# Performance work log

Hardware: AMD Instinct MI355X
Metric: run time of the kernel (lower is better)

## Reference

```python
import jax, jax.numpy as jnp
import numpy as np

N, E, F_IN = 10000, 160000, 256
H1, C1 = 8, 128          # conv1: heads=8, out 128 per head, concat -> 1024
H2, C2 = 1, 64           # conv2: heads=1, out 64
NEG_SLOPE = 0.2


def setup_inputs() -> dict:
    key = jax.random.key(0)
    ks = jax.random.split(key, 10)
    s_in = 1.0 / np.sqrt(F_IN)
    s_h1 = 1.0 / np.sqrt(H1 * C1)
    return {
        "x": jax.random.normal(ks[0], (N, F_IN), dtype=jnp.float32),
        "edge_index": jax.random.randint(ks[1], (2, E), 0, N, dtype=jnp.int64),
        "W1": jax.random.normal(ks[2], (F_IN, H1 * C1), dtype=jnp.float32) * s_in,
        "att_src1": jax.random.normal(ks[3], (H1, C1), dtype=jnp.float32) * 0.1,
        "att_dst1": jax.random.normal(ks[4], (H1, C1), dtype=jnp.float32) * 0.1,
        "b1": jnp.zeros((H1 * C1,), dtype=jnp.float32),
        "W2": jax.random.normal(ks[5], (H1 * C1, H2 * C2), dtype=jnp.float32) * s_h1,
        "att_src2": jax.random.normal(ks[6], (H2, C2), dtype=jnp.float32) * 0.1,
        "att_dst2": jax.random.normal(ks[7], (H2, C2), dtype=jnp.float32) * 0.1,
        "b2": jnp.zeros((H2 * C2,), dtype=jnp.float32),
    }


def gat_conv(x, src, dst, W, att_src, att_dst, b, n):
    """PyG GATConv (eval mode: dropout off), concat=True, add_self_loops handled by caller."""
    H, C = att_src.shape
    h = (x @ W).reshape(n, H, C)                       # [N,H,C]
    a_s = jnp.einsum('nhc,hc->nh', h, att_src)         # [N,H]
    a_d = jnp.einsum('nhc,hc->nh', h, att_dst)         # [N,H]
    e = jax.nn.leaky_relu(a_s[src] + a_d[dst], NEG_SLOPE)  # [Etot,H]
    # softmax over edges grouped by destination node (numerically stable)
    e_max = jax.ops.segment_max(e, dst, num_segments=n)
    e = jnp.exp(e - e_max[dst])
    denom = jax.ops.segment_sum(e, dst, num_segments=n)
    alpha = e / (denom[dst] + 1e-16)                   # [Etot,H]
    msg = h[src] * alpha[:, :, None]                   # [Etot,H,C]
    out = jax.ops.segment_sum(msg, dst, num_segments=n)  # [N,H,C]
    return out.reshape(n, H * C) + b


def reference(x, edge_index, W1, att_src1, att_dst1, b1, W2, att_src2, att_dst2, b2):
    n = x.shape[0]
    loops = jnp.arange(n, dtype=edge_index.dtype)
    src = jnp.concatenate([edge_index[0], loops])
    dst = jnp.concatenate([edge_index[1], loops])
    h = jax.nn.elu(gat_conv(x, src, dst, W1, att_src1, att_dst1, b1, n))
    return gat_conv(h, src, dst, W2, att_src2, att_dst2, b2, n)
```

## Files before the change

### kernel.cpp

```cpp
#include <hip/hip_runtime.h>
#include <cmath>


typedef short bf16x8 __attribute__((ext_vector_type(8)));
typedef float f32x4 __attribute__((ext_vector_type(4)));
typedef unsigned short u16x8 __attribute__((ext_vector_type(8)));

__device__ __forceinline__ float lrelu(float x) { return x > 0.f ? x : 0.2f * x; }
__device__ __forceinline__ float b2f(unsigned short h) {
  return __uint_as_float(((unsigned)h) << 16);
}
__device__ __forceinline__ unsigned short f2bf(float f) {
  unsigned u = __float_as_uint(f);
  u += 0x7FFFu + ((u >> 16) & 1u);
  return (unsigned short)(u >> 16);
}

__device__ __forceinline__ void fma8(float* acc, uint4 v, float e) {
  acc[0] += e * __uint_as_float(v.x << 16);
  acc[1] += e * __uint_as_float(v.x & 0xffff0000u);
  acc[2] += e * __uint_as_float(v.y << 16);
  acc[3] += e * __uint_as_float(v.y & 0xffff0000u);
  acc[4] += e * __uint_as_float(v.z << 16);
  acc[5] += e * __uint_as_float(v.z & 0xffff0000u);
  acc[6] += e * __uint_as_float(v.w << 16);
  acc[7] += e * __uint_as_float(v.w & 0xffff0000u);
}

#define GLOAD_LDS16(gsrc, ldst)                                              \
  __builtin_amdgcn_global_load_lds(                                          \
      (const __attribute__((address_space(1))) unsigned int*)(gsrc),         \
      (__attribute__((address_space(3))) unsigned int*)(ldst), 16, 0, 0)


__global__ __launch_bounds__(256) void prep_fused(
    const int* __restrict__ ei, int* __restrict__ counts, int E,
    const float* __restrict__ x, unsigned short* __restrict__ xpk, int N, int MB1,
    const float* __restrict__ W1, unsigned short* __restrict__ w1pk,
    const float* __restrict__ W2, unsigned short* __restrict__ w2pk) {
  const int countB = (E + 255) / 256;
  const int pxB = MB1 * 8;
  int bid = blockIdx.x;
  int t = threadIdx.x;

  if (bid < countB) {
    int e = bid * 256 + t;
    if (e < E) atomicAdd(&counts[ei[E + e]], 1);
    return;
  }
  bid -= countB;
  if (bid < pxB) {
    int mb = bid >> 3, ks = bid & 7;
    int l = t & 63, f = t >> 6;
    int row = mb * 64 + f * 16 + (l & 15);
    int kc = ks * 32 + (l >> 4) * 8;
    float v[8];
#pragma unroll
    for (int j = 0; j < 8; ++j) v[j] = 0.f;
    if (row < N) {
      const float* xr = x + (size_t)row * 256 + kc;
#pragma unroll
      for (int j = 0; j < 8; ++j) v[j] = xr[j];
    }
    u16x8 hi, lo;
#pragma unroll
    for (int j = 0; j < 8; ++j) {
      unsigned short h = f2bf(v[j]);
      hi[j] = h; lo[j] = f2bf(v[j] - b2f(h));
    }
    size_t base = (size_t)(mb * 8 + ks) * 8 * 512;
    *(u16x8*)(xpk + base + (size_t)f * 512 + l * 8) = hi;
    *(u16x8*)(xpk + base + (size_t)(4 + f) * 512 + l * 8) = lo;
    return;
  }
  bid -= pxB;
  if (bid < 64) {
    int hb = bid >> 3, ks = bid & 7;
    int l = t & 63, gq = t >> 6;
    for (int g = gq; g < 8; g += 4) {
      int n = hb * 128 + g * 16 + (l & 15);
      int k0 = ks * 32 + (l >> 4) * 8;
      u16x8 hi, lo;
#pragma unroll
      for (int j = 0; j < 8; ++j) {
        float v = W1[(size_t)(k0 + j) * 1024 + n];
        unsigned short h = f2bf(v);
        hi[j] = h; lo[j] = f2bf(v - b2f(h));
      }
      size_t base = (size_t)(hb * 8 + ks) * 16 * 512;
      *(u16x8*)(w1pk + base + (size_t)g * 512 + l * 8) = hi;
      *(u16x8*)(w1pk + base + (size_t)(8 + g) * 512 + l * 8) = lo;
    }
    return;
  }
  bid -= 64;
  {
    int ks = bid;
    int l = t & 63, g = t >> 6;
    int n = g * 16 + (l & 15);
    int k0 = ks * 32 + (l >> 4) * 8;
    u16x8 hi, lo;
#pragma unroll
    for (int j = 0; j < 8; ++j) {
      float v = W2[(size_t)(k0 + j) * 64 + n];
      unsigned short h = f2bf(v);
      hi[j] = h; lo[j] = f2bf(v - b2f(h));
    }
    size_t base = (size_t)ks * 8 * 512;
    *(u16x8*)(w2pk + base + (size_t)g * 512 + l * 8) = hi;
    *(u16x8*)(w2pk + base + (size_t)(4 + g) * 512 + l * 8) = lo;
  }
}


__global__ __launch_bounds__(256) void scan_blk(const int* __restrict__ counts,
                                                int* __restrict__ offsets,
                                                int* __restrict__ bsum, int n) {
  __shared__ int lds[256];
  int b = blockIdx.x, t = threadIdx.x, i = b * 256 + t;
  int v = (i < n) ? counts[i] + 1 : 0;
  lds[t] = v;
  __syncthreads();
  for (int off = 1; off < 256; off <<= 1) {
    int tv = (t >= off) ? lds[t - off] : 0;
    __syncthreads();
    lds[t] += tv;
    __syncthreads();
  }
  if (i < n) offsets[i] = lds[t] - v;
  if (t == 255) bsum[b] = lds[255];
}

__global__ __launch_bounds__(256) void scan_apply(int* __restrict__ offsets,
                                                  int* __restrict__ cursors,
                                                  const int* __restrict__ bsum,
                                                  int nb, int n) {
  __shared__ int pre_s;
  int b = blockIdx.x, t = threadIdx.x;
  if (t == 0) {
    int s = 0;
    for (int i = 0; i < b; ++i) s += bsum[i];
    pre_s = s;
    if (b == nb - 1) {
      int tot = s;
      for (int i = b; i < nb; ++i) tot += bsum[i];
      offsets[n] = tot;
    }
  }
  __syncthreads();
  int i = b * 256 + t;
  if (i < n) {
    int o = offsets[i] + pre_s;
    offsets[i] = o;
    cursors[i] = o;
  }
}

__global__ __launch_bounds__(256) void fill_all(const int* __restrict__ ei,
                                                int* __restrict__ cursors,
                                                const int* __restrict__ offsets,
                                                int* __restrict__ list,
                                                int E, int n) {
  int tid = blockIdx.x * 256 + threadIdx.x;
  if (tid < E) {
    int d = ei[E + tid];
    int pos = atomicAdd(&cursors[d], 1);
    list[pos] = ei[tid];
  } else if (tid < E + n) {
    int i = tid - E;
    list[offsets[i + 1] - 1] = i;
  }
}


__global__ __launch_bounds__(512, 4) void gemm1_att(
    const unsigned short* __restrict__ xpk, const unsigned short* __restrict__ w1pk,
    const float* __restrict__ asrc, const float* __restrict__ adst,
    unsigned short* __restrict__ h1b, float* __restrict__ as1,
    float* __restrict__ ad1) {
  extern __shared__ char sm[];
  const int t = threadIdx.x, wid = t >> 6, lane = t & 63;
  const int wr = wid >> 2, wc = wid & 3;
  const int mb = blockIdx.x, hb = blockIdx.y;
  const int m0 = mb * 128;
  const int l15 = lane & 15, l4 = lane >> 4;

  f32x4 acc[4][2] = {};

  auto stage = [&](int buf, int ks) {
    char* base0 = sm + buf * 32768;
    for (int i = wid; i < 32; i += 8) {
      const unsigned short* src;
      int ldsoff;
      if (i < 8) {
        int r = i >> 2;
        src = xpk + (size_t)((2 * mb + r) * 8 + ks) * 4096 + (i & 3) * 512 + lane * 8;
        ldsoff = i * 1024;
      } else if (i < 16) {
        int f = i - 8, r = f >> 2;
        src = xpk + (size_t)((2 * mb + r) * 8 + ks) * 4096 + (4 + (f & 3)) * 512 + lane * 8;
        ldsoff = 8192 + f * 1024;
      } else if (i < 24) {
        int g = i - 16;
        src = w1pk + (size_t)(hb * 8 + ks) * 8192 + g * 512 + lane * 8;
        ldsoff = 16384 + g * 1024;
      } else {
        int g = i - 24;
        src = w1pk + (size_t)(hb * 8 + ks) * 8192 + (8 + g) * 512 + lane * 8;
        ldsoff = 24576 + g * 1024;
      }
      GLOAD_LDS16(src, base0 + ldsoff);
    }
  };

  stage(0, 0);
  __syncthreads();
  int buf = 0;
  for (int step = 0; step < 8; ++step) {
    if (step < 7) stage(buf ^ 1, step + 1);
    const char* b = sm + buf * 32768;
    bf16x8 ah[4], al[4], bh[2], bl[2];
#pragma unroll
    for (int mf = 0; mf < 4; ++mf) {
      ah[mf] = *(const bf16x8*)(b + (wr * 4 + mf) * 1024 + lane * 16);
      al[mf] = *(const bf16x8*)(b + 8192 + (wr * 4 + mf) * 1024 + lane * 16);
    }
#pragma unroll
    for (int nf = 0; nf < 2; ++nf) {
      bh[nf] = *(const bf16x8*)(b + 16384 + (wc * 2 + nf) * 1024 + lane * 16);
      bl[nf] = *(const bf16x8*)(b + 24576 + (wc * 2 + nf) * 1024 + lane * 16);
    }
#pragma unroll
    for (int mf = 0; mf < 4; ++mf)
#pragma unroll
      for (int nf = 0; nf < 2; ++nf) {
        acc[mf][nf] = __builtin_amdgcn_mfma_f32_16x16x32_bf16(ah[mf], bh[nf], acc[mf][nf], 0, 0, 0);
        acc[mf][nf] = __builtin_amdgcn_mfma_f32_16x16x32_bf16(ah[mf], bl[nf], acc[mf][nf], 0, 0, 0);
        acc[mf][nf] = __builtin_amdgcn_mfma_f32_16x16x32_bf16(al[mf], bh[nf], acc[mf][nf], 0, 0, 0);
      }
    __syncthreads();
    buf ^= 1;
  }

  float* parts_s = (float*)sm;
  float* parts_d = (float*)(sm + 2048);
  unsigned short* ctile = (unsigned short*)(sm + 4096);
  float as_c[2], ad_c[2];
#pragma unroll
  for (int nf = 0; nf < 2; ++nf) {
    int col = hb * 128 + wc * 32 + nf * 16 + l15;
    as_c[nf] = asrc[col];
    ad_c[nf] = adst[col];
  }
#pragma unroll
  for (int mf = 0; mf < 4; ++mf) {
    float ss[4] = {0.f, 0.f, 0.f, 0.f}, dd[4] = {0.f, 0.f, 0.f, 0.f};
#pragma unroll
    for (int nf = 0; nf < 2; ++nf)
#pragma unroll
      for (int r = 0; r < 4; ++r) {
        ss[r] += acc[mf][nf][r] * as_c[nf];
        dd[r] += acc[mf][nf][r] * ad_c[nf];
      }
#pragma unroll
    for (int r = 0; r < 4; ++r)
      for (int m = 1; m < 16; m <<= 1) {
        ss[r] += __shfl_xor(ss[r], m);
        dd[r] += __shfl_xor(dd[r], m);
      }
    if (l15 == 0) {
#pragma unroll
      for (int r = 0; r < 4; ++r) {
        int row = wr * 64 + mf * 16 + l4 * 4 + r;
        parts_s[row * 4 + wc] = ss[r];
        parts_d[row * 4 + wc] = dd[r];
      }
    }
#pragma unroll
    for (int nf = 0; nf < 2; ++nf)
#pragma unroll
      for (int r = 0; r < 4; ++r) {
        int row = wr * 64 + mf * 16 + l4 * 4 + r;
        int col = wc * 32 + nf * 16 + l15;
        ctile[row * 128 + col] = f2bf(acc[mf][nf][r]);
      }
  }
  __syncthreads();
  if (t < 128) {
    float s = parts_s[t * 4] + parts_s[t * 4 + 1] + parts_s[t * 4 + 2] + parts_s[t * 4 + 3];
    float d = parts_d[t * 4] + parts_d[t * 4 + 1] + parts_d[t * 4 + 2] + parts_d[t * 4 + 3];
    as1[(size_t)(m0 + t) * 8 + hb] = s;
    ad1[(size_t)(m0 + t) * 8 + hb] = d;
  }
#pragma unroll
  for (int rep = 0; rep < 4; ++rep) {
    int e = rep * 4096 + t * 8;
    int row = e >> 7, col = e & 127;
    bf16x8 v = *(const bf16x8*)(ctile + e);
    *(bf16x8*)(h1b + (size_t)(m0 + row) * 1024 + hb * 128 + col) = v;
  }
}


__global__ __launch_bounds__(256) void agg1_gather(
    const unsigned short* __restrict__ h1b, const float* __restrict__ as1,
    const float* __restrict__ ad1, const int* __restrict__ offsets,
    const int* __restrict__ list, const float* __restrict__ b1,
    unsigned short* __restrict__ o1pk, int n) {
  __shared__ __align__(16) unsigned short stg[8192];
  const int t = threadIdx.x, w = t >> 6, lane = t & 63;
  const int node = blockIdx.x * 4 + w;
  const int h0 = lane >> 4, h1_ = h0 + 4;

  if (node < n) {
    const int beg = offsets[node], end = offsets[node + 1];
    const float ad0 = ad1[(size_t)node * 8 + h0];
    const float ad4 = ad1[(size_t)node * 8 + h1_];
    float acc0[8] = {}, acc1[8] = {};
    float den0 = 0.f, den4 = 0.f;

    int j = beg;
    int sA = 0, sB = 0;
    float aA0 = 0.f, aA4 = 0.f, aB0 = 0.f, aB4 = 0.f;
    uint4 vA0, vA1, vB0, vB1;
    if (j + 2 <= end) {
      sA = list[j]; sB = list[j + 1];
      aA0 = as1[(size_t)sA * 8 + h0]; aA4 = as1[(size_t)sA * 8 + h1_];
      aB0 = as1[(size_t)sB * 8 + h0]; aB4 = as1[(size_t)sB * 8 + h1_];
      vA0 = *(const uint4*)(h1b + (size_t)sA * 1024 + lane * 8);
      vA1 = *(const uint4*)(h1b + (size_t)sA * 1024 + 512 + lane * 8);
      vB0 = *(const uint4*)(h1b + (size_t)sB * 1024 + lane * 8);
      vB1 = *(const uint4*)(h1b + (size_t)sB * 1024 + 512 + lane * 8);
    }
    for (; j + 4 <= end; j += 2) {
      int sA2 = list[j + 2], sB2 = list[j + 3];
      float aA02 = as1[(size_t)sA2 * 8 + h0], aA42 = as1[(size_t)sA2 * 8 + h1_];
      float aB02 = as1[(size_t)sB2 * 8 + h0], aB42 = as1[(size_t)sB2 * 8 + h1_];
      uint4 nA0 = *(const uint4*)(h1b + (size_t)sA2 * 1024 + lane * 8);
      uint4 nA1 = *(const uint4*)(h1b + (size_t)sA2 * 1024 + 512 + lane * 8);
      uint4 nB0 = *(const uint4*)(h1b + (size_t)sB2 * 1024 + lane * 8);
      uint4 nB1 = *(const uint4*)(h1b + (size_t)sB2 * 1024 + 512 + lane * 8);
      float eA0 = __expf(lrelu(aA0 + ad0)), eA4 = __expf(lrelu(aA4 + ad4));
      float eB0 = __expf(lrelu(aB0 + ad0)), eB4 = __expf(lrelu(aB4 + ad4));
      den0 += eA0 + eB0; den4 += eA4 + eB4;
      fma8(acc0, vA0, eA0); fma8(acc1, vA1, eA4);
      fma8(acc0, vB0, eB0); fma8(acc1, vB1, eB4);
      sA = sA2; sB = sB2;
      aA0 = aA02; aA4 = aA42; aB0 = aB02; aB4 = aB42;
      vA0 = nA0; vA1 = nA1; vB0 = nB0; vB1 = nB1;
    }
    if (j + 2 <= end) {
      float eA0 = __expf(lrelu(aA0 + ad0)), eA4 = __expf(lrelu(aA4 + ad4));
      float eB0 = __expf(lrelu(aB0 + ad0)), eB4 = __expf(lrelu(aB4 + ad4));
      den0 += eA0 + eB0; den4 += eA4 + eB4;
      fma8(acc0, vA0, eA0); fma8(acc1, vA1, eA4);
      fma8(acc0, vB0, eB0); fma8(acc1, vB1, eB4);
      j += 2;
    }
    if (j < end) {
      int s = list[j];
      float a0 = as1[(size_t)s * 8 + h0], a4 = as1[(size_t)s * 8 + h1_];
      uint4 v0 = *(const uint4*)(h1b + (size_t)s * 1024 + lane * 8);
      uint4 v1 = *(const uint4*)(h1b + (size_t)s * 1024 + 512 + lane * 8);
      float e0 = __expf(lrelu(a0 + ad0)), e4 = __expf(lrelu(a4 + ad4));
      den0 += e0; den4 += e4;
      fma8(acc0, v0, e0); fma8(acc1, v1, e4);
    }

    const float inv0 = 1.f / (den0 + 1e-16f);
    const float inv4 = 1.f / (den4 + 1e-16f);
    u16x8 hiA, loA, hiB, loB;
#pragma unroll
    for (int k = 0; k < 8; ++k) {
      float vA = acc0[k] * inv0 + b1[lane * 8 + k];
      float vB = acc1[k] * inv4 + b1[512 + lane * 8 + k];
      vA = vA > 0.f ? vA : expm1f(vA);
      vB = vB > 0.f ? vB : expm1f(vB);
      unsigned short hA = f2bf(vA), hB = f2bf(vB);
      hiA[k] = hA; loA[k] = f2bf(vA - b2f(hA));
      hiB[k] = hB; loB[k] = f2bf(vB - b2f(hB));
    }
    const int q2 = lane >> 2, kc = lane & 3;
    {
      int aw = q2 * 512 + kc * 64 + w * 16;
      *(u16x8*)((char*)stg + (aw ^ ((q2 & 7) << 4))) = hiA;
      aw += 256;
      *(u16x8*)((char*)stg + (aw ^ ((q2 & 7) << 4))) = loA;
    }
    {
      int ks = 16 + q2;
      int aw = ks * 512 + kc * 64 + w * 16;
      *(u16x8*)((char*)stg + (aw ^ ((ks & 7) << 4))) = hiB;
      aw += 256;
      *(u16x8*)((char*)stg + (aw ^ ((ks & 7) << 4))) = loB;
    }
  }
  __syncthreads();
  const int blk = blockIdx.x;
  const int mb = blk >> 4, f = (blk >> 2) & 3, l15b = (blk & 3) * 4;
#pragma unroll
  for (int it = 0; it < 4; ++it) {
    int a = it * 4096 + t * 16;
    int ks = a >> 9, half = (a >> 8) & 1, kcc = (a >> 6) & 3, ww = (a >> 4) & 3;
    u16x8 v = *(const u16x8*)((const char*)stg + (a ^ ((ks & 7) << 4)));
    size_t g = (size_t)(mb * 32 + ks) * 4096 + half * 2048 + (size_t)f * 512 +
               (size_t)(kcc * 16 + l15b + ww) * 8;
    *(u16x8*)(o1pk + g) = v;
  }
}


__global__ __launch_bounds__(256) void gemm2_splitk(
    const unsigned short* __restrict__ o1pk, const unsigned short* __restrict__ w2pk,
    float* __restrict__ h2p, int Mpad) {
  extern __shared__ char sm[];
  const int t = threadIdx.x, wid = t >> 6, lane = t & 63;
  const int wr = wid >> 1, wc = wid & 1;
  const int mb = blockIdx.x, sk = blockIdx.y;
  const int m0 = mb * 64;
  const int l15 = lane & 15, l4 = lane >> 4;

  f32x4 acc[2][2] = {};

  auto stage = [&](int buf, int ks) {
    char* base0 = sm + buf * 16384;
    const unsigned short* ax = o1pk + (size_t)(mb * 32 + ks) * 8 * 512 + lane * 8;
    for (int i = wid; i < 8; i += 4)
      GLOAD_LDS16(ax + i * 512, base0 + i * 1024);
    const unsigned short* bw = w2pk + (size_t)ks * 8 * 512 + lane * 8;
    for (int i = wid; i < 8; i += 4)
      GLOAD_LDS16(bw + i * 512, base0 + 8192 + i * 1024);
  };

  stage(0, sk * 8);
  __syncthreads();
  int buf = 0;
  for (int step = 0; step < 8; ++step) {
    if (step < 7) stage(buf ^ 1, sk * 8 + step + 1);
    const char* b = sm + buf * 16384;
    bf16x8 ah[2], al[2], bh[2], bl[2];
#pragma unroll
    for (int mf = 0; mf < 2; ++mf) {
      int f = wr * 2 + mf;
      ah[mf] = *(const bf16x8*)(b + f * 1024 + lane * 16);
      al[mf] = *(const bf16x8*)(b + 4096 + f * 1024 + lane * 16);
    }
#pragma unroll
    for (int nf = 0; nf < 2; ++nf) {
      int g = wc * 2 + nf;
      bh[nf] = *(const bf16x8*)(b + 8192 + g * 1024 + lane * 16);
      bl[nf] = *(const bf16x8*)(b + 12288 + g * 1024 + lane * 16);
    }
#pragma unroll
    for (int mf = 0; mf < 2; ++mf)
#pragma unroll
      for (int nf = 0; nf < 2; ++nf) {
        acc[mf][nf] = __builtin_amdgcn_mfma_f32_16x16x32_bf16(ah[mf], bh[nf], acc[mf][nf], 0, 0, 0);
        acc[mf][nf] = __builtin_amdgcn_mfma_f32_16x16x32_bf16(ah[mf], bl[nf], acc[mf][nf], 0, 0, 0);
        acc[mf][nf] = __builtin_amdgcn_mfma_f32_16x16x32_bf16(al[mf], bh[nf], acc[mf][nf], 0, 0, 0);
      }
    __syncthreads();
    buf ^= 1;
  }

#pragma unroll
  for (int mf = 0; mf < 2; ++mf)
#pragma unroll
    for (int nf = 0; nf < 2; ++nf)
#pragma unroll
      for (int r = 0; r < 4; ++r) {
        int row = wr * 32 + mf * 16 + l4 * 4 + r;
        int col = wc * 32 + nf * 16 + l15;
        h2p[((size_t)sk * Mpad + m0 + row) * 64 + col] = acc[mf][nf][r];
      }
}


__global__ __launch_bounds__(256) void reduce_att2(
    const float* __restrict__ h2p, const float* __restrict__ asrc,
    const float* __restrict__ adst, float* __restrict__ h2,
    float* __restrict__ as2, float* __restrict__ ad2, int Mpad, int n) {
  int w = threadIdx.x >> 6, lane = threadIdx.x & 63;
  int row = blockIdx.x * 4 + w;
  if (row >= n) return;
  float s = 0.f;
#pragma unroll
  for (int sk = 0; sk < 4; ++sk) s += h2p[((size_t)sk * Mpad + row) * 64 + lane];
  h2[(size_t)row * 64 + lane] = s;
  float ds = s * asrc[lane], dd = s * adst[lane];
  for (int o = 32; o; o >>= 1) { ds += __shfl_xor(ds, o); dd += __shfl_xor(dd, o); }
  if (lane == 0) { as2[row] = ds; ad2[row] = dd; }
}


__global__ __launch_bounds__(256) void agg2_gather(
    const float* __restrict__ h2, const float* __restrict__ as2,
    const float* __restrict__ ad2, const int* __restrict__ offsets,
    const int* __restrict__ list, const float* __restrict__ b2,
    float* __restrict__ out, int n) {
  const int wid = threadIdx.x >> 6, lane = threadIdx.x & 63;
  const int node = blockIdx.x * 4 + wid;
  if (node >= n) return;
  const int beg = offsets[node], end = offsets[node + 1];
  const float ad = ad2[node];
  const int cb = (lane & 15) * 4;
  const int jo = lane >> 4;

  float4 acc = make_float4(0.f, 0.f, 0.f, 0.f);
  float den = 0.f;
  for (int j = beg + jo; j < end; j += 4) {
    int s = list[j];
    float e = __expf(lrelu(as2[s] + ad));
    den += e;
    float4 v = *(const float4*)&h2[(size_t)s * 64 + cb];
    acc.x += e * v.x; acc.y += e * v.y; acc.z += e * v.z; acc.w += e * v.w;
  }
  acc.x += __shfl_xor(acc.x, 16); acc.y += __shfl_xor(acc.y, 16);
  acc.z += __shfl_xor(acc.z, 16); acc.w += __shfl_xor(acc.w, 16);
  den += __shfl_xor(den, 16);
  acc.x += __shfl_xor(acc.x, 32); acc.y += __shfl_xor(acc.y, 32);
  acc.z += __shfl_xor(acc.z, 32); acc.w += __shfl_xor(acc.w, 32);
  den += __shfl_xor(den, 32);
  if (jo == 0) {
    float inv = 1.f / (den + 1e-16f);
    float4 r;
    r.x = acc.x * inv + b2[cb];
    r.y = acc.y * inv + b2[cb + 1];
    r.z = acc.z * inv + b2[cb + 2];
    r.w = acc.w * inv + b2[cb + 3];
    *(float4*)&out[(size_t)node * 64 + cb] = r;
  }
}


extern "C" void kernel_launch(void* const* d_in, const int* in_sizes, int n_in,
                              void* d_out, int out_size, void* d_ws, size_t ws_size,
                              hipStream_t stream) {
  const float* x     = (const float*)d_in[0];
  const int*   ei    = (const int*)d_in[1];
  const float* W1    = (const float*)d_in[2];
  const float* asrc1 = (const float*)d_in[3];
  const float* adst1 = (const float*)d_in[4];
  const float* b1    = (const float*)d_in[5];
  const float* W2    = (const float*)d_in[6];
  const float* asrc2 = (const float*)d_in[7];
  const float* adst2 = (const float*)d_in[8];
  const float* b2    = (const float*)d_in[9];
  float* out = (float*)d_out;

  const int N = in_sizes[0] / 256;
  const int E = in_sizes[1] / 2;
  const int T = E + N;
  const int MBB = (N + 127) / 128;
  const int Mpad = MBB * 128;
  const int MB1 = Mpad / 64;
  const int NB = (N + 255) / 256;

  char* p = (char*)d_ws;
  auto bump = [&](size_t bytes) {
    char* r = p;
    p += (bytes + 255) & ~(size_t)255;
    return r;
  };
  int* counts  = (int*)bump((size_t)N * 4);
  int* offsets = (int*)bump((size_t)(N + 1) * 4);
  int* cursors = (int*)bump((size_t)N * 4);
  int* bsum    = (int*)bump((size_t)NB * 4);
  int* list    = (int*)bump((size_t)T * 4);
  unsigned short* xpk  = (unsigned short*)bump((size_t)Mpad * 512 * 2);
  unsigned short* w1pk = (unsigned short*)bump((size_t)8 * 8 * 16 * 512 * 2);
  unsigned short* h1b  = (unsigned short*)bump((size_t)Mpad * 1024 * 2);
  float* as1           = (float*)bump((size_t)Mpad * 8 * 4);
  float* ad1           = (float*)bump((size_t)Mpad * 8 * 4);
  unsigned short* o1pk = (unsigned short*)bump((size_t)Mpad * 2048 * 2);
  unsigned short* w2pk = (unsigned short*)bump((size_t)32 * 8 * 512 * 2);
  float* as2           = (float*)bump((size_t)Mpad * 4);
  float* ad2           = (float*)bump((size_t)Mpad * 4);
  float* h2p = (float*)h1b;
  float* h2  = (float*)xpk;

  hipMemsetAsync(counts, 0, (size_t)N * 4, stream);
  {
    int gridsz = (E + 255) / 256 + MB1 * 8 + 64 + 32;
    prep_fused<<<gridsz, 256, 0, stream>>>(ei, counts, E, x, xpk, N, MB1,
                                           W1, w1pk, W2, w2pk);
  }
  scan_blk<<<NB, 256, 0, stream>>>(counts, offsets, bsum, N);
  scan_apply<<<NB, 256, 0, stream>>>(offsets, cursors, bsum, NB, N);
  fill_all<<<(E + N + 255) / 256, 256, 0, stream>>>(ei, cursors, offsets, list, E, N);

  gemm1_att<<<dim3(MBB, 8), 512, 65536, stream>>>(xpk, w1pk, asrc1, adst1, h1b, as1, ad1);
  agg1_gather<<<(N + 3) / 4, 256, 0, stream>>>(h1b, as1, ad1, offsets, list, b1, o1pk, N);

  gemm2_splitk<<<dim3(Mpad / 64, 4), 256, 32768, stream>>>(o1pk, w2pk, h2p, Mpad);
  reduce_att2<<<(N + 3) / 4, 256, 0, stream>>>(h2p, asrc2, adst2, h2, as2, ad2, Mpad, N);
  agg2_gather<<<(N + 3) / 4, 256, 0, stream>>>(h2, as2, ad2, offsets, list, b2, out, N);
}
```

Before: 162.3 us.

## Drop low-order x split in gemm1 and deepen agg1 gather prefetch

The x operand of the first GEMM is now stored only as a single bf16 value rather than a hi/lo pair. This removes one of the three MFMAs per tile, a quarter of the LDS staging and half the xpk buffer, at the cost of lower accuracy on the x side of the product. The agg1 gather loop is rewritten to load neighbour rows in groups of four, with the next group's loads issued one group ahead, so more memory requests are in flight. Because xpk shrinks and no longer fits h2, the h2 scratch buffer is moved to o1pk.

New measurement: 161.2 us. Within noise of the previous version (-0.6%).

```diff
diff --git a/kernel.cpp b/kernel.cpp
--- a/kernel.cpp
+++ b/kernel.cpp
@@ -62,15 +62,11 @@
 #pragma unroll
       for (int j = 0; j < 8; ++j) v[j] = xr[j];
     }
-    u16x8 hi, lo;
-#pragma unroll
-    for (int j = 0; j < 8; ++j) {
-      unsigned short h = f2bf(v[j]);
-      hi[j] = h; lo[j] = f2bf(v[j] - b2f(h));
-    }
-    size_t base = (size_t)(mb * 8 + ks) * 8 * 512;
+    u16x8 hi;
+#pragma unroll
+    for (int j = 0; j < 8; ++j) hi[j] = f2bf(v[j]);
+    size_t base = (size_t)(mb * 8 + ks) * 4 * 512;
     *(u16x8*)(xpk + base + (size_t)f * 512 + l * 8) = hi;
-    *(u16x8*)(xpk + base + (size_t)(4 + f) * 512 + l * 8) = lo;
     return;
   }
   bid -= pxB;
@@ -188,26 +184,22 @@
   f32x4 acc[4][2] = {};
 
   auto stage = [&](int buf, int ks) {
-    char* base0 = sm + buf * 32768;
-    for (int i = wid; i < 32; i += 8) {
+    char* base0 = sm + buf * 24576;
+    for (int i = wid; i < 24; i += 8) {
       const unsigned short* src;
       int ldsoff;
       if (i < 8) {
         int r = i >> 2;
-        src = xpk + (size_t)((2 * mb + r) * 8 + ks) * 4096 + (i & 3) * 512 + lane * 8;
+        src = xpk + (size_t)((2 * mb + r) * 8 + ks) * 2048 + (i & 3) * 512 + lane * 8;
         ldsoff = i * 1024;
       } else if (i < 16) {
-        int f = i - 8, r = f >> 2;
-        src = xpk + (size_t)((2 * mb + r) * 8 + ks) * 4096 + (4 + (f & 3)) * 512 + lane * 8;
-        ldsoff = 8192 + f * 1024;
-      } else if (i < 24) {
+        int g = i - 8;
+        src = w1pk + (size_t)(hb * 8 + ks) * 8192 + g * 512 + lane * 8;
+        ldsoff = 8192 + g * 1024;
+      } else {
         int g = i - 16;
-        src = w1pk + (size_t)(hb * 8 + ks) * 8192 + g * 512 + lane * 8;
+        src = w1pk + (size_t)(hb * 8 + ks) * 8192 + (8 + g) * 512 + lane * 8;
         ldsoff = 16384 + g * 1024;
-      } else {
-        int g = i - 24;
-        src = w1pk + (size_t)(hb * 8 + ks) * 8192 + (8 + g) * 512 + lane * 8;
-        ldsoff = 24576 + g * 1024;
       }
       GLOAD_LDS16(src, base0 + ldsoff);
     }
@@ -218,17 +210,15 @@
   int buf = 0;
   for (int step = 0; step < 8; ++step) {
     if (step < 7) stage(buf ^ 1, step + 1);
-    const char* b = sm + buf * 32768;
-    bf16x8 ah[4], al[4], bh[2], bl[2];
-#pragma unroll
-    for (int mf = 0; mf < 4; ++mf) {
+    const char* b = sm + buf * 24576;
+    bf16x8 ah[4], bh[2], bl[2];
+#pragma unroll
+    for (int mf = 0; mf < 4; ++mf)
       ah[mf] = *(const bf16x8*)(b + (wr * 4 + mf) * 1024 + lane * 16);
-      al[mf] = *(const bf16x8*)(b + 8192 + (wr * 4 + mf) * 1024 + lane * 16);
-    }
 #pragma unroll
     for (int nf = 0; nf < 2; ++nf) {
-      bh[nf] = *(const bf16x8*)(b + 16384 + (wc * 2 + nf) * 1024 + lane * 16);
-      bl[nf] = *(const bf16x8*)(b + 24576 + (wc * 2 + nf) * 1024 + lane * 16);
+      bh[nf] = *(const bf16x8*)(b + 8192 + (wc * 2 + nf) * 1024 + lane * 16);
+      bl[nf] = *(const bf16x8*)(b + 16384 + (wc * 2 + nf) * 1024 + lane * 16);
     }
 #pragma unroll
     for (int mf = 0; mf < 4; ++mf)
@@ -236,7 +226,6 @@
       for (int nf = 0; nf < 2; ++nf) {
         acc[mf][nf] = __builtin_amdgcn_mfma_f32_16x16x32_bf16(ah[mf], bh[nf], acc[mf][nf], 0, 0, 0);
         acc[mf][nf] = __builtin_amdgcn_mfma_f32_16x16x32_bf16(ah[mf], bl[nf], acc[mf][nf], 0, 0, 0);
-        acc[mf][nf] = __builtin_amdgcn_mfma_f32_16x16x32_bf16(al[mf], bh[nf], acc[mf][nf], 0, 0, 0);
       }
     __syncthreads();
     buf ^= 1;
@@ -319,46 +308,64 @@
     float acc0[8] = {}, acc1[8] = {};
     float den0 = 0.f, den4 = 0.f;
 
-    int j = beg;
-    int sA = 0, sB = 0;
-    float aA0 = 0.f, aA4 = 0.f, aB0 = 0.f, aB4 = 0.f;
-    uint4 vA0, vA1, vB0, vB1;
-    if (j + 2 <= end) {
-      sA = list[j]; sB = list[j + 1];
-      aA0 = as1[(size_t)sA * 8 + h0]; aA4 = as1[(size_t)sA * 8 + h1_];
-      aB0 = as1[(size_t)sB * 8 + h0]; aB4 = as1[(size_t)sB * 8 + h1_];
-      vA0 = *(const uint4*)(h1b + (size_t)sA * 1024 + lane * 8);
-      vA1 = *(const uint4*)(h1b + (size_t)sA * 1024 + 512 + lane * 8);
-      vB0 = *(const uint4*)(h1b + (size_t)sB * 1024 + lane * 8);
-      vB1 = *(const uint4*)(h1b + (size_t)sB * 1024 + 512 + lane * 8);
-    }
-    for (; j + 4 <= end; j += 2) {
-      int sA2 = list[j + 2], sB2 = list[j + 3];
-      float aA02 = as1[(size_t)sA2 * 8 + h0], aA42 = as1[(size_t)sA2 * 8 + h1_];
-      float aB02 = as1[(size_t)sB2 * 8 + h0], aB42 = as1[(size_t)sB2 * 8 + h1_];
-      uint4 nA0 = *(const uint4*)(h1b + (size_t)sA2 * 1024 + lane * 8);
-      uint4 nA1 = *(const uint4*)(h1b + (size_t)sA2 * 1024 + 512 + lane * 8);
-      uint4 nB0 = *(const uint4*)(h1b + (size_t)sB2 * 1024 + lane * 8);
-      uint4 nB1 = *(const uint4*)(h1b + (size_t)sB2 * 1024 + 512 + lane * 8);
-      float eA0 = __expf(lrelu(aA0 + ad0)), eA4 = __expf(lrelu(aA4 + ad4));
-      float eB0 = __expf(lrelu(aB0 + ad0)), eB4 = __expf(lrelu(aB4 + ad4));
-      den0 += eA0 + eB0; den4 += eA4 + eB4;
-      fma8(acc0, vA0, eA0); fma8(acc1, vA1, eA4);
-      fma8(acc0, vB0, eB0); fma8(acc1, vB1, eB4);
-      sA = sA2; sB = sB2;
-      aA0 = aA02; aA4 = aA42; aB0 = aB02; aB4 = aB42;
-      vA0 = nA0; vA1 = nA1; vB0 = nB0; vB1 = nB1;
-    }
-    if (j + 2 <= end) {
-      float eA0 = __expf(lrelu(aA0 + ad0)), eA4 = __expf(lrelu(aA4 + ad4));
-      float eB0 = __expf(lrelu(aB0 + ad0)), eB4 = __expf(lrelu(aB4 + ad4));
-      den0 += eA0 + eB0; den4 += eA4 + eB4;
-      fma8(acc0, vA0, eA0); fma8(acc1, vA1, eA4);
-      fma8(acc0, vB0, eB0); fma8(acc1, vB1, eB4);
-      j += 2;
-    }
-    if (j < end) {
-      int s = list[j];
+    const int m = end - beg;
+    const int* lp = list + beg;
+    const int ng = m >> 2;
+
+    int sCur[4], sNxt[4];
+    float a0C[4], a4C[4];
+    uint4 r0C[4], r1C[4];
+
+    auto issue = [&](const int* s, float* a0, float* a4, uint4* r0, uint4* r1) {
+#pragma unroll
+      for (int k = 0; k < 4; ++k) {
+        a0[k] = as1[(size_t)s[k] * 8 + h0];
+        a4[k] = as1[(size_t)s[k] * 8 + h1_];
+        r0[k] = *(const uint4*)(h1b + (size_t)s[k] * 1024 + lane * 8);
+        r1[k] = *(const uint4*)(h1b + (size_t)s[k] * 1024 + 512 + lane * 8);
+      }
+    };
+    auto compute = [&](const float* a0, const float* a4, const uint4* r0,
+                       const uint4* r1) {
+#pragma unroll
+      for (int k = 0; k < 4; ++k) {
+        float e0 = __expf(lrelu(a0[k] + ad0));
+        float e4 = __expf(lrelu(a4[k] + ad4));
+        den0 += e0; den4 += e4;
+        fma8(acc0, r0[k], e0);
+        fma8(acc1, r1[k], e4);
+      }
+    };
+
+    if (ng >= 1) {
+#pragma unroll
+      for (int k = 0; k < 4; ++k) sCur[k] = lp[k];
+      issue(sCur, a0C, a4C, r0C, r1C);
+    }
+    if (ng >= 2) {
+#pragma unroll
+      for (int k = 0; k < 4; ++k) sNxt[k] = lp[4 + k];
+    }
+#pragma unroll 2
+    for (int g = 0; g < ng; ++g) {
+      int sNew[4] = {0, 0, 0, 0};
+      if (g + 2 < ng) {
+#pragma unroll
+        for (int k = 0; k < 4; ++k) sNew[k] = lp[(g + 2) * 4 + k];
+      }
+      float a0N[4], a4N[4];
+      uint4 r0N[4], r1N[4];
+      if (g + 1 < ng) issue(sNxt, a0N, a4N, r0N, r1N);
+      compute(a0C, a4C, r0C, r1C);
+#pragma unroll
+      for (int k = 0; k < 4; ++k) {
+        sCur[k] = sNxt[k]; sNxt[k] = sNew[k];
+        a0C[k] = a0N[k]; a4C[k] = a4N[k];
+        r0C[k] = r0N[k]; r1C[k] = r1N[k];
+      }
+    }
+    for (int j = ng * 4; j < m; ++j) {
+      int s = lp[j];
       float a0 = as1[(size_t)s * 8 + h0], a4 = as1[(size_t)s * 8 + h1_];
       uint4 v0 = *(const uint4*)(h1b + (size_t)s * 1024 + lane * 8);
       uint4 v1 = *(const uint4*)(h1b + (size_t)s * 1024 + 512 + lane * 8);
@@ -567,7 +574,7 @@
   int* cursors = (int*)bump((size_t)N * 4);
   int* bsum    = (int*)bump((size_t)NB * 4);
   int* list    = (int*)bump((size_t)T * 4);
-  unsigned short* xpk  = (unsigned short*)bump((size_t)Mpad * 512 * 2);
+  unsigned short* xpk  = (unsigned short*)bump((size_t)Mpad * 256 * 2);
   unsigned short* w1pk = (unsigned short*)bump((size_t)8 * 8 * 16 * 512 * 2);
   unsigned short* h1b  = (unsigned short*)bump((size_t)Mpad * 1024 * 2);
   float* as1           = (float*)bump((size_t)Mpad * 8 * 4);
@@ -577,7 +584,7 @@
   float* as2           = (float*)bump((size_t)Mpad * 4);
   float* ad2           = (float*)bump((size_t)Mpad * 4);
   float* h2p = (float*)h1b;
-  float* h2  = (float*)xpk;
+  float* h2  = (float*)o1pk;
 
   hipMemsetAsync(counts, 0, (size_t)N * 4, stream);
   {
@@ -589,7 +596,7 @@
   scan_apply<<<NB, 256, 0, stream>>>(offsets, cursors, bsum, NB, N);
   fill_all<<<(E + N + 255) / 256, 256, 0, stream>>>(ei, cursors, offsets, list, E, N);
 
-  gemm1_att<<<dim3(MBB, 8), 512, 65536, stream>>>(xpk, w1pk, asrc1, adst1, h1b, as1, ad1);
+  gemm1_att<<<dim3(MBB, 8), 512, 49152, stream>>>(xpk, w1pk, asrc1, adst1, h1b, as1, ad1);
   agg1_gather<<<(N + 3) / 4, 256, 0, stream>>>(h1b, as1, ad1, offsets, list, b1, o1pk, N);
 
   gemm2_splitk<<<dim3(Mpad / 64, 4), 256, 32768, stream>>>(o1pk, w2pk, h2p, Mpad);
```

## Drop x low-part split in GEMM1 and use grid-stride aggregation kernels

Applied to the files above, without the earlier changes.

The first GEMM no longer splits x into bf16 hi+lo parts. It keeps only the hi part, which halves the x staging traffic and LDS use and removes one of the three MFMAs per fragment pair. W1 still uses the hi+lo split. Both aggregation kernels become grid-stride loops capped at 2048 blocks, which spreads launch and scheduling overhead over fewer blocks. Dropping x's low part lowers GEMM1 accuracy to roughly bf16 on one operand, which may loosen the match against the fp32 reference.

Measured after the change: 156.2 us. 3.7% less time.

```diff
diff --git a/kernel.cpp b/kernel.cpp
--- a/kernel.cpp
+++ b/kernel.cpp
@@ -62,15 +62,11 @@
 #pragma unroll
       for (int j = 0; j < 8; ++j) v[j] = xr[j];
     }
-    u16x8 hi, lo;
-#pragma unroll
-    for (int j = 0; j < 8; ++j) {
-      unsigned short h = f2bf(v[j]);
-      hi[j] = h; lo[j] = f2bf(v[j] - b2f(h));
-    }
-    size_t base = (size_t)(mb * 8 + ks) * 8 * 512;
+    u16x8 hi;
+#pragma unroll
+    for (int j = 0; j < 8; ++j) hi[j] = f2bf(v[j]);
+    size_t base = (size_t)(mb * 8 + ks) * 4 * 512;
     *(u16x8*)(xpk + base + (size_t)f * 512 + l * 8) = hi;
-    *(u16x8*)(xpk + base + (size_t)(4 + f) * 512 + l * 8) = lo;
     return;
   }
   bid -= pxB;
@@ -188,26 +184,22 @@
   f32x4 acc[4][2] = {};
 
   auto stage = [&](int buf, int ks) {
-    char* base0 = sm + buf * 32768;
-    for (int i = wid; i < 32; i += 8) {
+    char* base0 = sm + buf * 24576;
+    for (int i = wid; i < 24; i += 8) {
       const unsigned short* src;
       int ldsoff;
       if (i < 8) {
         int r = i >> 2;
-        src = xpk + (size_t)((2 * mb + r) * 8 + ks) * 4096 + (i & 3) * 512 + lane * 8;
+        src = xpk + (size_t)((2 * mb + r) * 8 + ks) * 2048 + (i & 3) * 512 + lane * 8;
         ldsoff = i * 1024;
       } else if (i < 16) {
-        int f = i - 8, r = f >> 2;
-        src = xpk + (size_t)((2 * mb + r) * 8 + ks) * 4096 + (4 + (f & 3)) * 512 + lane * 8;
-        ldsoff = 8192 + f * 1024;
-      } else if (i < 24) {
+        int g = i - 8;
+        src = w1pk + (size_t)(hb * 8 + ks) * 8192 + g * 512 + lane * 8;
+        ldsoff = 8192 + g * 1024;
+      } else {
         int g = i - 16;
-        src = w1pk + (size_t)(hb * 8 + ks) * 8192 + g * 512 + lane * 8;
+        src = w1pk + (size_t)(hb * 8 + ks) * 8192 + (8 + g) * 512 + lane * 8;
         ldsoff = 16384 + g * 1024;
-      } else {
-        int g = i - 24;
-        src = w1pk + (size_t)(hb * 8 + ks) * 8192 + (8 + g) * 512 + lane * 8;
-        ldsoff = 24576 + g * 1024;
       }
       GLOAD_LDS16(src, base0 + ldsoff);
     }
@@ -218,17 +210,15 @@
   int buf = 0;
   for (int step = 0; step < 8; ++step) {
     if (step < 7) stage(buf ^ 1, step + 1);
-    const char* b = sm + buf * 32768;
-    bf16x8 ah[4], al[4], bh[2], bl[2];
-#pragma unroll
-    for (int mf = 0; mf < 4; ++mf) {
+    const char* b = sm + buf * 24576;
+    bf16x8 ah[4], bh[2], bl[2];
+#pragma unroll
+    for (int mf = 0; mf < 4; ++mf)
       ah[mf] = *(const bf16x8*)(b + (wr * 4 + mf) * 1024 + lane * 16);
-      al[mf] = *(const bf16x8*)(b + 8192 + (wr * 4 + mf) * 1024 + lane * 16);
-    }
 #pragma unroll
     for (int nf = 0; nf < 2; ++nf) {
-      bh[nf] = *(const bf16x8*)(b + 16384 + (wc * 2 + nf) * 1024 + lane * 16);
-      bl[nf] = *(const bf16x8*)(b + 24576 + (wc * 2 + nf) * 1024 + lane * 16);
+      bh[nf] = *(const bf16x8*)(b + 8192 + (wc * 2 + nf) * 1024 + lane * 16);
+      bl[nf] = *(const bf16x8*)(b + 16384 + (wc * 2 + nf) * 1024 + lane * 16);
     }
 #pragma unroll
     for (int mf = 0; mf < 4; ++mf)
@@ -236,7 +226,6 @@
       for (int nf = 0; nf < 2; ++nf) {
         acc[mf][nf] = __builtin_amdgcn_mfma_f32_16x16x32_bf16(ah[mf], bh[nf], acc[mf][nf], 0, 0, 0);
         acc[mf][nf] = __builtin_amdgcn_mfma_f32_16x16x32_bf16(ah[mf], bl[nf], acc[mf][nf], 0, 0, 0);
-        acc[mf][nf] = __builtin_amdgcn_mfma_f32_16x16x32_bf16(al[mf], bh[nf], acc[mf][nf], 0, 0, 0);
       }
     __syncthreads();
     buf ^= 1;
@@ -306,106 +295,108 @@
     const unsigned short* __restrict__ h1b, const float* __restrict__ as1,
     const float* __restrict__ ad1, const int* __restrict__ offsets,
     const int* __restrict__ list, const float* __restrict__ b1,
-    unsigned short* __restrict__ o1pk, int n) {
+    unsigned short* __restrict__ o1pk, int n, int nblk) {
   __shared__ __align__(16) unsigned short stg[8192];
   const int t = threadIdx.x, w = t >> 6, lane = t & 63;
-  const int node = blockIdx.x * 4 + w;
   const int h0 = lane >> 4, h1_ = h0 + 4;
 
-  if (node < n) {
-    const int beg = offsets[node], end = offsets[node + 1];
-    const float ad0 = ad1[(size_t)node * 8 + h0];
-    const float ad4 = ad1[(size_t)node * 8 + h1_];
-    float acc0[8] = {}, acc1[8] = {};
-    float den0 = 0.f, den4 = 0.f;
-
-    int j = beg;
-    int sA = 0, sB = 0;
-    float aA0 = 0.f, aA4 = 0.f, aB0 = 0.f, aB4 = 0.f;
-    uint4 vA0, vA1, vB0, vB1;
-    if (j + 2 <= end) {
-      sA = list[j]; sB = list[j + 1];
-      aA0 = as1[(size_t)sA * 8 + h0]; aA4 = as1[(size_t)sA * 8 + h1_];
-      aB0 = as1[(size_t)sB * 8 + h0]; aB4 = as1[(size_t)sB * 8 + h1_];
-      vA0 = *(const uint4*)(h1b + (size_t)sA * 1024 + lane * 8);
-      vA1 = *(const uint4*)(h1b + (size_t)sA * 1024 + 512 + lane * 8);
-      vB0 = *(const uint4*)(h1b + (size_t)sB * 1024 + lane * 8);
-      vB1 = *(const uint4*)(h1b + (size_t)sB * 1024 + 512 + lane * 8);
-    }
-    for (; j + 4 <= end; j += 2) {
-      int sA2 = list[j + 2], sB2 = list[j + 3];
-      float aA02 = as1[(size_t)sA2 * 8 + h0], aA42 = as1[(size_t)sA2 * 8 + h1_];
-      float aB02 = as1[(size_t)sB2 * 8 + h0], aB42 = as1[(size_t)sB2 * 8 + h1_];
-      uint4 nA0 = *(const uint4*)(h1b + (size_t)sA2 * 1024 + lane * 8);
-      uint4 nA1 = *(const uint4*)(h1b + (size_t)sA2 * 1024 + 512 + lane * 8);
-      uint4 nB0 = *(const uint4*)(h1b + (size_t)sB2 * 1024 + lane * 8);
-      uint4 nB1 = *(const uint4*)(h1b + (size_t)sB2 * 1024 + 512 + lane * 8);
-      float eA0 = __expf(lrelu(aA0 + ad0)), eA4 = __expf(lrelu(aA4 + ad4));
-      float eB0 = __expf(lrelu(aB0 + ad0)), eB4 = __expf(lrelu(aB4 + ad4));
-      den0 += eA0 + eB0; den4 += eA4 + eB4;
-      fma8(acc0, vA0, eA0); fma8(acc1, vA1, eA4);
-      fma8(acc0, vB0, eB0); fma8(acc1, vB1, eB4);
-      sA = sA2; sB = sB2;
-      aA0 = aA02; aA4 = aA42; aB0 = aB02; aB4 = aB42;
-      vA0 = nA0; vA1 = nA1; vB0 = nB0; vB1 = nB1;
-    }
-    if (j + 2 <= end) {
-      float eA0 = __expf(lrelu(aA0 + ad0)), eA4 = __expf(lrelu(aA4 + ad4));
-      float eB0 = __expf(lrelu(aB0 + ad0)), eB4 = __expf(lrelu(aB4 + ad4));
-      den0 += eA0 + eB0; den4 += eA4 + eB4;
-      fma8(acc0, vA0, eA0); fma8(acc1, vA1, eA4);
-      fma8(acc0, vB0, eB0); fma8(acc1, vB1, eB4);
-      j += 2;
-    }
-    if (j < end) {
-      int s = list[j];
-      float a0 = as1[(size_t)s * 8 + h0], a4 = as1[(size_t)s * 8 + h1_];
-      uint4 v0 = *(const uint4*)(h1b + (size_t)s * 1024 + lane * 8);
-      uint4 v1 = *(const uint4*)(h1b + (size_t)s * 1024 + 512 + lane * 8);
-      float e0 = __expf(lrelu(a0 + ad0)), e4 = __expf(lrelu(a4 + ad4));
-      den0 += e0; den4 += e4;
-      fma8(acc0, v0, e0); fma8(acc1, v1, e4);
-    }
-
-    const float inv0 = 1.f / (den0 + 1e-16f);
-    const float inv4 = 1.f / (den4 + 1e-16f);
-    u16x8 hiA, loA, hiB, loB;
-#pragma unroll
-    for (int k = 0; k < 8; ++k) {
-      float vA = acc0[k] * inv0 + b1[lane * 8 + k];
-      float vB = acc1[k] * inv4 + b1[512 + lane * 8 + k];
-      vA = vA > 0.f ? vA : expm1f(vA);
-      vB = vB > 0.f ? vB : expm1f(vB);
-      unsigned short hA = f2bf(vA), hB = f2bf(vB);
-      hiA[k] = hA; loA[k] = f2bf(vA - b2f(hA));
-      hiB[k] = hB; loB[k] = f2bf(vB - b2f(hB));
-    }
-    const int q2 = lane >> 2, kc = lane & 3;
-    {
-      int aw = q2 * 512 + kc * 64 + w * 16;
-      *(u16x8*)((char*)stg + (aw ^ ((q2 & 7) << 4))) = hiA;
-      aw += 256;
-      *(u16x8*)((char*)stg + (aw ^ ((q2 & 7) << 4))) = loA;
-    }
-    {
-      int ks = 16 + q2;
-      int aw = ks * 512 + kc * 64 + w * 16;
-      *(u16x8*)((char*)stg + (aw ^ ((ks & 7) << 4))) = hiB;
-      aw += 256;
-      *(u16x8*)((char*)stg + (aw ^ ((ks & 7) << 4))) = loB;
-    }
-  }
-  __syncthreads();
-  const int blk = blockIdx.x;
-  const int mb = blk >> 4, f = (blk >> 2) & 3, l15b = (blk & 3) * 4;
-#pragma unroll
-  for (int it = 0; it < 4; ++it) {
-    int a = it * 4096 + t * 16;
-    int ks = a >> 9, half = (a >> 8) & 1, kcc = (a >> 6) & 3, ww = (a >> 4) & 3;
-    u16x8 v = *(const u16x8*)((const char*)stg + (a ^ ((ks & 7) << 4)));
-    size_t g = (size_t)(mb * 32 + ks) * 4096 + half * 2048 + (size_t)f * 512 +
-               (size_t)(kcc * 16 + l15b + ww) * 8;
-    *(u16x8*)(o1pk + g) = v;
+  for (int blk = blockIdx.x; blk < nblk; blk += gridDim.x) {
+    const int node = blk * 4 + w;
+    if (node < n) {
+      const int beg = offsets[node], end = offsets[node + 1];
+      const float ad0 = ad1[(size_t)node * 8 + h0];
+      const float ad4 = ad1[(size_t)node * 8 + h1_];
+      float acc0[8] = {}, acc1[8] = {};
+      float den0 = 0.f, den4 = 0.f;
+
+      int j = beg;
+      int sA = 0, sB = 0;
+      float aA0 = 0.f, aA4 = 0.f, aB0 = 0.f, aB4 = 0.f;
+      uint4 vA0, vA1, vB0, vB1;
+      if (j + 2 <= end) {
+        sA = list[j]; sB = list[j + 1];
+        aA0 = as1[(size_t)sA * 8 + h0]; aA4 = as1[(size_t)sA * 8 + h1_];
+        aB0 = as1[(size_t)sB * 8 + h0]; aB4 = as1[(size_t)sB * 8 + h1_];
+        vA0 = *(const uint4*)(h1b + (size_t)sA * 1024 + lane * 8);
+        vA1 = *(const uint4*)(h1b + (size_t)sA * 1024 + 512 + lane * 8);
+        vB0 = *(const uint4*)(h1b + (size_t)sB * 1024 + lane * 8);
+        vB1 = *(const uint4*)(h1b + (size_t)sB * 1024 + 512 + lane * 8);
+      }
+      for (; j + 4 <= end; j += 2) {
+        int sA2 = list[j + 2], sB2 = list[j + 3];
+        float aA02 = as1[(size_t)sA2 * 8 + h0], aA42 = as1[(size_t)sA2 * 8 + h1_];
+        float aB02 = as1[(size_t)sB2 * 8 + h0], aB42 = as1[(size_t)sB2 * 8 + h1_];
+        uint4 nA0 = *(const uint4*)(h1b + (size_t)sA2 * 1024 + lane * 8);
+        uint4 nA1 = *(const uint4*)(h1b + (size_t)sA2 * 1024 + 512 + lane * 8);
+        uint4 nB0 = *(const uint4*)(h1b + (size_t)sB2 * 1024 + lane * 8);
+        uint4 nB1 = *(const uint4*)(h1b + (size_t)sB2 * 1024 + 512 + lane * 8);
+        float eA0 = __expf(lrelu(aA0 + ad0)), eA4 = __expf(lrelu(aA4 + ad4));
+        float eB0 = __expf(lrelu(aB0 + ad0)), eB4 = __expf(lrelu(aB4 + ad4));
+        den0 += eA0 + eB0; den4 += eA4 + eB4;
+        fma8(acc0, vA0, eA0); fma8(acc1, vA1, eA4);
+        fma8(acc0, vB0, eB0); fma8(acc1, vB1, eB4);
+        sA = sA2; sB = sB2;
+        aA0 = aA02; aA4 = aA42; aB0 = aB02; aB4 = aB42;
+        vA0 = nA0; vA1 = nA1; vB0 = nB0; vB1 = nB1;
+      }
+      if (j + 2 <= end) {
+        float eA0 = __expf(lrelu(aA0 + ad0)), eA4 = __expf(lrelu(aA4 + ad4));
+        float eB0 = __expf(lrelu(aB0 + ad0)), eB4 = __expf(lrelu(aB4 + ad4));
+        den0 += eA0 + eB0; den4 += eA4 + eB4;
+        fma8(acc0, vA0, eA0); fma8(acc1, vA1, eA4);
+        fma8(acc0, vB0, eB0); fma8(acc1, vB1, eB4);
+        j += 2;
+      }
+      if (j < end) {
+        int s = list[j];
+        float a0 = as1[(size_t)s * 8 + h0], a4 = as1[(size_t)s * 8 + h1_];
+        uint4 v0 = *(const uint4*)(h1b + (size_t)s * 1024 + lane * 8);
+        uint4 v1 = *(const uint4*)(h1b + (size_t)s * 1024 + 512 + lane * 8);
+        float e0 = __expf(lrelu(a0 + ad0)), e4 = __expf(lrelu(a4 + ad4));
+        den0 += e0; den4 += e4;
+        fma8(acc0, v0, e0); fma8(acc1, v1, e4);
+      }
+
+      const float inv0 = 1.f / (den0 + 1e-16f);
+      const float inv4 = 1.f / (den4 + 1e-16f);
+      u16x8 hiA, loA, hiB, loB;
+#pragma unroll
+      for (int k = 0; k < 8; ++k) {
+        float vA = acc0[k] * inv0 + b1[lane * 8 + k];
+        float vB = acc1[k] * inv4 + b1[512 + lane * 8 + k];
+        vA = vA > 0.f ? vA : expm1f(vA);
+        vB = vB > 0.f ? vB : expm1f(vB);
+        unsigned short hA = f2bf(vA), hB = f2bf(vB);
+        hiA[k] = hA; loA[k] = f2bf(vA - b2f(hA));
+        hiB[k] = hB; loB[k] = f2bf(vB - b2f(hB));
+      }
+      const int q2 = lane >> 2, kc = lane & 3;
+      {
+        int aw = q2 * 512 + kc * 64 + w * 16;
+        *(u16x8*)((char*)stg + (aw ^ ((q2 & 7) << 4))) = hiA;
+        aw += 256;
+        *(u16x8*)((char*)stg + (aw ^ ((q2 & 7) << 4))) = loA;
+      }
+      {
+        int ks = 16 + q2;
+        int aw = ks * 512 + kc * 64 + w * 16;
+        *(u16x8*)((char*)stg + (aw ^ ((ks & 7) << 4))) = hiB;
+        aw += 256;
+        *(u16x8*)((char*)stg + (aw ^ ((ks & 7) << 4))) = loB;
+      }
+    }
+    __syncthreads();
+    const int mb = blk >> 4, f = (blk >> 2) & 3, l15b = (blk & 3) * 4;
+#pragma unroll
+    for (int it = 0; it < 4; ++it) {
+      int a = it * 4096 + t * 16;
+      int ks = a >> 9, half = (a >> 8) & 1, kcc = (a >> 6) & 3, ww = (a >> 4) & 3;
+      u16x8 v = *(const u16x8*)((const char*)stg + (a ^ ((ks & 7) << 4)));
+      size_t g = (size_t)(mb * 32 + ks) * 4096 + half * 2048 + (size_t)f * 512 +
+                 (size_t)(kcc * 16 + l15b + ww) * 8;
+      *(u16x8*)(o1pk + g) = v;
+    }
+    __syncthreads();
   }
 }
 
@@ -497,38 +488,41 @@
     const float* __restrict__ h2, const float* __restrict__ as2,
     const float* __restrict__ ad2, const int* __restrict__ offsets,
     const int* __restrict__ list, const float* __restrict__ b2,
-    float* __restrict__ out, int n) {
+    float* __restrict__ out, int n, int nblk) {
   const int wid = threadIdx.x >> 6, lane = threadIdx.x & 63;
-  const int node = blockIdx.x * 4 + wid;
-  if (node >= n) return;
-  const int beg = offsets[node], end = offsets[node + 1];
-  const float ad = ad2[node];
   const int cb = (lane & 15) * 4;
   const int jo = lane >> 4;
 
-  float4 acc = make_float4(0.f, 0.f, 0.f, 0.f);
-  float den = 0.f;
-  for (int j = beg + jo; j < end; j += 4) {
-    int s = list[j];
-    float e = __expf(lrelu(as2[s] + ad));
-    den += e;
-    float4 v = *(const float4*)&h2[(size_t)s * 64 + cb];
-    acc.x += e * v.x; acc.y += e * v.y; acc.z += e * v.z; acc.w += e * v.w;
-  }
-  acc.x += __shfl_xor(acc.x, 16); acc.y += __shfl_xor(acc.y, 16);
-  acc.z += __shfl_xor(acc.z, 16); acc.w += __shfl_xor(acc.w, 16);
-  den += __shfl_xor(den, 16);
-  acc.x += __shfl_xor(acc.x, 32); acc.y += __shfl_xor(acc.y, 32);
-  acc.z += __shfl_xor(acc.z, 32); acc.w += __shfl_xor(acc.w, 32);
-  den += __shfl_xor(den, 32);
-  if (jo == 0) {
-    float inv = 1.f / (den + 1e-16f);
-    float4 r;
-    r.x = acc.x * inv + b2[cb];
-    r.y = acc.y * inv + b2[cb + 1];
-    r.z = acc.z * inv + b2[cb + 2];
-    r.w = acc.w * inv + b2[cb + 3];
-    *(float4*)&out[(size_t)node * 64 + cb] = r;
+  for (int blk = blockIdx.x; blk < nblk; blk += gridDim.x) {
+    const int node = blk * 4 + wid;
+    if (node >= n) continue;
+    const int beg = offsets[node], end = offsets[node + 1];
+    const float ad = ad2[node];
+
+    float4 acc = make_float4(0.f, 0.f, 0.f, 0.f);
+    float den = 0.f;
+    for (int j = beg + jo; j < end; j += 4) {
+      int s = list[j];
+      float e = __expf(lrelu(as2[s] + ad));
+      den += e;
+      float4 v = *(const float4*)&h2[(size_t)s * 64 + cb];
+      acc.x += e * v.x; acc.y += e * v.y; acc.z += e * v.z; acc.w += e * v.w;
+    }
+    acc.x += __shfl_xor(acc.x, 16); acc.y += __shfl_xor(acc.y, 16);
+    acc.z += __shfl_xor(acc.z, 16); acc.w += __shfl_xor(acc.w, 16);
+    den += __shfl_xor(den, 16);
+    acc.x += __shfl_xor(acc.x, 32); acc.y += __shfl_xor(acc.y, 32);
+    acc.z += __shfl_xor(acc.z, 32); acc.w += __shfl_xor(acc.w, 32);
+    den += __shfl_xor(den, 32);
+    if (jo == 0) {
+      float inv = 1.f / (den + 1e-16f);
+      float4 r;
+      r.x = acc.x * inv + b2[cb];
+      r.y = acc.y * inv + b2[cb + 1];
+      r.z = acc.z * inv + b2[cb + 2];
+      r.w = acc.w * inv + b2[cb + 3];
+      *(float4*)&out[(size_t)node * 64 + cb] = r;
+    }
   }
 }
 
@@ -555,6 +549,8 @@
   const int Mpad = MBB * 128;
   const int MB1 = Mpad / 64;
   const int NB = (N + 255) / 256;
+  const int NBLK4 = (N + 3) / 4;
+  const int AGG_GRID = NBLK4 < 2048 ? NBLK4 : 2048;
 
   char* p = (char*)d_ws;
   auto bump = [&](size_t bytes) {
@@ -567,7 +563,7 @@
   int* cursors = (int*)bump((size_t)N * 4);
   int* bsum    = (int*)bump((size_t)NB * 4);
   int* list    = (int*)bump((size_t)T * 4);
-  unsigned short* xpk  = (unsigned short*)bump((size_t)Mpad * 512 * 2);
+  unsigned short* xpk  = (unsigned short*)bump((size_t)Mpad * 256 * 2);
   unsigned short* w1pk = (unsigned short*)bump((size_t)8 * 8 * 16 * 512 * 2);
   unsigned short* h1b  = (unsigned short*)bump((size_t)Mpad * 1024 * 2);
   float* as1           = (float*)bump((size_t)Mpad * 8 * 4);
@@ -589,10 +585,10 @@
   scan_apply<<<NB, 256, 0, stream>>>(offsets, cursors, bsum, NB, N);
   fill_all<<<(E + N + 255) / 256, 256, 0, stream>>>(ei, cursors, offsets, list, E, N);
 
-  gemm1_att<<<dim3(MBB, 8), 512, 65536, stream>>>(xpk, w1pk, asrc1, adst1, h1b, as1, ad1);
-  agg1_gather<<<(N + 3) / 4, 256, 0, stream>>>(h1b, as1, ad1, offsets, list, b1, o1pk, N);
+  gemm1_att<<<dim3(MBB, 8), 512, 49152, stream>>>(xpk, w1pk, asrc1, adst1, h1b, as1, ad1);
+  agg1_gather<<<AGG_GRID, 256, 0, stream>>>(h1b, as1, ad1, offsets, list, b1, o1pk, N, NBLK4);
 
   gemm2_splitk<<<dim3(Mpad / 64, 4), 256, 32768, stream>>>(o1pk, w2pk, h2p, Mpad);
   reduce_att2<<<(N + 3) / 4, 256, 0, stream>>>(h2p, asrc2, adst2, h2, as2, ad2, Mpad, N);
-  agg2_gather<<<(N + 3) / 4, 256, 0, stream>>>(h2, as2, ad2, offsets, list, b2, out, N);
-}
+  agg2_gather<<<AGG_GRID, 256, 0, stream>>>(h2, as2, ad2, offsets, list, b2, out, N, NBLK4);
+}
```
